# Kernel optimization log

Hardware: AMD Instinct MI355X
Metric: run time of the kernel (lower is better)

The kernel has to match this reference:

```python
import jax, jax.numpy as jnp
import numpy as np

EMBED = 1024
HEADS = 16
HEAD_DIM = EMBED // HEADS


def setup_inputs() -> dict:
    key = jax.random.key(0)
    ks = jax.random.split(key, 8)
    N, L = 4, 2048
    values = jax.random.normal(ks[0], (N, L, EMBED), dtype=jnp.float32)
    keys_ = jax.random.normal(ks[1], (N, L, EMBED), dtype=jnp.float32)
    queries = jax.random.normal(ks[2], (N, L, EMBED), dtype=jnp.float32)
    s = 1.0 / np.sqrt(HEAD_DIM)
    Wv = jax.random.normal(ks[3], (HEAD_DIM, HEAD_DIM), dtype=jnp.float32) * s
    Wk = jax.random.normal(ks[4], (HEAD_DIM, HEAD_DIM), dtype=jnp.float32) * s
    Wq = jax.random.normal(ks[5], (HEAD_DIM, HEAD_DIM), dtype=jnp.float32) * s
    Wo = jax.random.normal(ks[6], (EMBED, EMBED), dtype=jnp.float32) * (1.0 / np.sqrt(EMBED))
    bo = jnp.zeros((EMBED,), dtype=jnp.float32)
    return {"values": values, "keys": keys_, "queries": queries,
            "Wv": Wv, "Wk": Wk, "Wq": Wq, "Wo": Wo, "bo": bo}


def reference(values, keys, queries, Wv, Wk, Wq, Wo, bo):
    N, L, _ = queries.shape
    # split heads: [N, L, H, D]
    v = values.reshape(N, -1, HEADS, HEAD_DIM)
    k = keys.reshape(N, -1, HEADS, HEAD_DIM)
    q = queries.reshape(N, L, HEADS, HEAD_DIM)
    # per-head linear (same [D,D] weight shared across heads), torch Linear: x @ W.T
    v = jnp.einsum('nlhd,ed->nlhe', v, Wv)
    k = jnp.einsum('nlhd,ed->nlhe', k, Wk)
    q = jnp.einsum('nqhd,ed->nqhe', q, Wq)
    # attention scores [N, H, Q, K], scaled by sqrt(embed_size) as in source
    scores = jnp.einsum('nqhd,nkhd->nhqk', q, k) / jnp.sqrt(jnp.float32(EMBED))
    attn = jax.nn.softmax(scores, axis=-1)
    out = jnp.einsum('nhqk,nkhd->nqhd', attn, v).reshape(N, L, EMBED)
    return out @ Wo.T + bo
```

## Files before the change

### kernel.cpp

```cpp
#include <hip/hip_runtime.h>
#include <math.h>

#define EMBED 1024
#define HEADS 16
#define HD    64
#define NB    4
#define LSEQ  2048

typedef __attribute__((ext_vector_type(8))) short bf16x8;
typedef __attribute__((ext_vector_type(16))) float f32x16;

typedef __attribute__((address_space(1))) void as1_void;
typedef __attribute__((address_space(3))) void as3_void;

__device__ __forceinline__ void gload_lds16(const void* g, void* l) {
    __builtin_amdgcn_global_load_lds((const as1_void*)g, (as3_void*)l, 16, 0, 0);
}

__device__ inline bf16x8 as_bf16x8(uint4 u) {
    union { uint4 u; bf16x8 b; } c; c.u = u; return c.b;
}
__device__ inline unsigned short bf16r(float x) {
    unsigned u = __float_as_uint(x);
    u += 0x7fffu + ((u >> 16) & 1u);
    return (unsigned short)(u >> 16);
}
__device__ inline float bfh2f(unsigned short h) {
    return __uint_as_float(((unsigned)h) << 16);
}
__device__ inline void split2(float x, float y, unsigned& hw, unsigned& lw) {
    unsigned short hx = bf16r(x), hy = bf16r(y);
    unsigned short lx = bf16r(x - bfh2f(hx)), ly = bf16r(y - bfh2f(hy));
    hw = (unsigned)hx | ((unsigned)hy << 16);
    lw = (unsigned)lx | ((unsigned)ly << 16);
}

__global__ __launch_bounds__(256, 3) void proj_kernel(
    const float* __restrict__ Xv, const float* __restrict__ Xk, const float* __restrict__ Xq,
    const float* __restrict__ Wv, const float* __restrict__ Wk, const float* __restrict__ Wq,
    unsigned short* __restrict__ Vt, unsigned short* __restrict__ Kp, unsigned short* __restrict__ Qp)
{
    __shared__ uint4 sXh[128 * 8];
    __shared__ uint4 sXl[128 * 8];
    __shared__ uint4 sWh[64 * 8];
    __shared__ uint4 sWl[64 * 8];

    const int t = threadIdx.x;
    const int lane = t & 63, w = t >> 6;
    const int l5 = lane & 31, hi = lane >> 5;
    const int h  = blockIdx.y;
    const int n  = blockIdx.x >> 4;
    const int l0 = (blockIdx.x & 15) * 128;
    const int p  = blockIdx.z;

    const float QSC = 1.44269504088896341f / 32.0f;
    const float* Xp = (p == 0) ? Xv : (p == 1) ? Xk : Xq;
    const float* Wp = (p == 0) ? Wv : (p == 1) ? Wk : Wq;

    const int frow = t >> 4;
    const int fcol = t & 15;

    {
        const float* xb = Xp + ((size_t)(n * LSEQ + l0 + frow)) * EMBED + h * HD + fcol * 4;
        unsigned short* dh = (unsigned short*)sXh;
        unsigned short* dl = (unsigned short*)sXl;
        #pragma unroll
        for (int i = 0; i < 8; ++i) {
            int row = frow + i * 16;
            float4 v = *(const float4*)(xb + (size_t)i * 16 * EMBED);
            int gg = fcol >> 1, s8 = (fcol & 1) * 4;
            int idx = row * 64 + ((gg ^ (row & 7)) * 8) + s8;
            uint2 hv, lv;
            split2(v.x, v.y, hv.x, lv.x);
            split2(v.z, v.w, hv.y, lv.y);
            *(uint2*)(dh + idx) = hv;
            *(uint2*)(dl + idx) = lv;
        }
    }
    #pragma unroll
    for (int i = 0; i < 2; ++i) {
        int u = t + 256 * i;
        int e = u >> 3, g = u & 7;
        const float* wb = Wp + u * 8;
        float4 v0 = *(const float4*)(wb);
        float4 v1 = *(const float4*)(wb + 4);
        uint4 hq, lq;
        split2(v0.x, v0.y, hq.x, lq.x);
        split2(v0.z, v0.w, hq.y, lq.y);
        split2(v1.x, v1.y, hq.z, lq.z);
        split2(v1.z, v1.w, hq.w, lq.w);
        int idx = e * 8 + (g ^ (e & 7));
        sWh[idx] = hq;
        sWl[idx] = lq;
    }
    __syncthreads();

    f32x16 acc0, acc1;
    #pragma unroll
    for (int i = 0; i < 16; ++i) { acc0[i] = 0.f; acc1[i] = 0.f; }

    const int xrow = w * 32 + l5;
    const int w0r = l5, w1r = 32 + l5;
    #pragma unroll
    for (int kc = 0; kc < 4; ++kc) {
        int gsel = kc * 2 + hi;
        bf16x8 xh = as_bf16x8(sXh[xrow * 8 + (gsel ^ (xrow & 7))]);
        bf16x8 xl = as_bf16x8(sXl[xrow * 8 + (gsel ^ (xrow & 7))]);
        bf16x8 wh0 = as_bf16x8(sWh[w0r * 8 + (gsel ^ (w0r & 7))]);
        bf16x8 wl0 = as_bf16x8(sWl[w0r * 8 + (gsel ^ (w0r & 7))]);
        bf16x8 wh1 = as_bf16x8(sWh[w1r * 8 + (gsel ^ (w1r & 7))]);
        bf16x8 wl1 = as_bf16x8(sWl[w1r * 8 + (gsel ^ (w1r & 7))]);
        if (p == 0) {
            acc0 = __builtin_amdgcn_mfma_f32_32x32x16_bf16(wh0, xh, acc0, 0, 0, 0);
            acc0 = __builtin_amdgcn_mfma_f32_32x32x16_bf16(wh0, xl, acc0, 0, 0, 0);
            acc0 = __builtin_amdgcn_mfma_f32_32x32x16_bf16(wl0, xh, acc0, 0, 0, 0);
            acc1 = __builtin_amdgcn_mfma_f32_32x32x16_bf16(wh1, xh, acc1, 0, 0, 0);
            acc1 = __builtin_amdgcn_mfma_f32_32x32x16_bf16(wh1, xl, acc1, 0, 0, 0);
            acc1 = __builtin_amdgcn_mfma_f32_32x32x16_bf16(wl1, xh, acc1, 0, 0, 0);
        } else {
            acc0 = __builtin_amdgcn_mfma_f32_32x32x16_bf16(xh, wh0, acc0, 0, 0, 0);
            acc0 = __builtin_amdgcn_mfma_f32_32x32x16_bf16(xh, wl0, acc0, 0, 0, 0);
            acc0 = __builtin_amdgcn_mfma_f32_32x32x16_bf16(xl, wh0, acc0, 0, 0, 0);
            acc1 = __builtin_amdgcn_mfma_f32_32x32x16_bf16(xh, wh1, acc1, 0, 0, 0);
            acc1 = __builtin_amdgcn_mfma_f32_32x32x16_bf16(xh, wl1, acc1, 0, 0, 0);
            acc1 = __builtin_amdgcn_mfma_f32_32x32x16_bf16(xl, wh1, acc1, 0, 0, 0);
        }
    }

    if (p == 0) {
        unsigned short* vb = Vt + (((size_t)(n * HEADS + h)) * HD) * LSEQ + l0 + w * 32 + l5;
        #pragma unroll
        for (int r = 0; r < 16; ++r) {
            int er = (r & 3) + 8 * (r >> 2) + 4 * hi;
            vb[(size_t)er * LSEQ]        = bf16r(acc0[r]);
            vb[(size_t)(32 + er) * LSEQ] = bf16r(acc1[r]);
        }
    } else {
        unsigned short* dst = (p == 1) ? Kp : Qp;
        float sc = (p == 2) ? QSC : 1.0f;
        unsigned short* db = dst + (((size_t)(n * HEADS + h)) * LSEQ + l0 + w * 32) * HD;
        #pragma unroll
        for (int r = 0; r < 16; ++r) {
            int tok = (r & 3) + 8 * (r >> 2) + 4 * hi;
            db[(size_t)tok * HD + l5]      = bf16r(acc0[r] * sc);
            db[(size_t)tok * HD + 32 + l5] = bf16r(acc1[r] * sc);
        }
    }
}

__global__ __launch_bounds__(256, 4) void attn_kernel(
    const unsigned short* __restrict__ Qp, const unsigned short* __restrict__ Kp,
    const unsigned short* __restrict__ Vt,
    unsigned short* __restrict__ AOh, unsigned short* __restrict__ AOl)
{
    __shared__ uint4 sK[2][64 * 8];
    __shared__ uint4 sV[2][64 * 8];

    const int t = threadIdx.x;
    const int lane = t & 63, w = t >> 6;
    const int l5 = lane & 31, hi = lane >> 5;
    const int n = blockIdx.z, h = blockIdx.y;
    const int q0 = blockIdx.x * 128;
    const size_t hoff = ((size_t)n * HEADS + h) * (size_t)(LSEQ * HD);
    const unsigned short* Kh = Kp + hoff;
    const unsigned short* Vh = Vt + hoff;

    bf16x8 qf[4];
    {
        const uint4* qg = (const uint4*)(Qp + hoff + (size_t)(q0 + w * 32 + l5) * HD);
        #pragma unroll
        for (int kc = 0; kc < 4; ++kc) qf[kc] = as_bf16x8(qg[kc * 2 + hi]);
    }

    f32x16 Oa0, Oa1;
    #pragma unroll
    for (int i = 0; i < 16; ++i) { Oa0[i] = 0.f; Oa1[i] = 0.f; }
    float ls0 = 0.f, ls1 = 0.f;

    const int r0 = t >> 3;
    const int g0 = (t & 7) ^ (r0 & 7);
    const uint4* gK = (const uint4*)Kh;
    const uint4* gV = (const uint4*)Vh;

    #define STAGE(TILE, BUF)                                                        \
        do {                                                                        \
            int kb_ = (TILE) * 64;                                                  \
            gload_lds16(gK + (size_t)(kb_ + r0) * 8 + g0,        &sK[BUF][t]);      \
            gload_lds16(gK + (size_t)(kb_ + r0 + 32) * 8 + g0,   &sK[BUF][t + 256]);\
            gload_lds16(gV + (size_t)r0 * 256 + (kb_ >> 3) + g0, &sV[BUF][t]);      \
            gload_lds16(gV + (size_t)(r0 + 32) * 256 + (kb_ >> 3) + g0,             \
                        &sV[BUF][t + 256]);                                         \
        } while (0)

    STAGE(0, 0);
    int cur = 0;

    for (int tt = 0; tt < LSEQ / 64; ++tt) {
        if (tt + 1 < LSEQ / 64) {
            STAGE(tt + 1, cur ^ 1);
            asm volatile("s_waitcnt vmcnt(4)" ::: "memory");
        } else {
            asm volatile("s_waitcnt vmcnt(0)" ::: "memory");
        }
        __builtin_amdgcn_s_barrier();

        #pragma unroll
        for (int tc = 0; tc < 2; ++tc) {
            f32x16 c;
            #pragma unroll
            for (int i = 0; i < 16; ++i) c[i] = 0.f;
            int key = tc * 32 + l5;
            __builtin_amdgcn_s_setprio(1);
            #pragma unroll
            for (int kc = 0; kc < 4; ++kc) {
                bf16x8 kf = as_bf16x8(sK[cur][key * 8 + ((kc * 2 + hi) ^ (l5 & 7))]);
                c = __builtin_amdgcn_mfma_f32_32x32x16_bf16(kf, qf[kc], c, 0, 0, 0);
            }
            __builtin_amdgcn_s_setprio(0);

            unsigned pw[8];
            #pragma unroll
            for (int g = 0; g < 4; ++g) {
                float p0 = exp2f(c[4 * g]);
                float p1 = exp2f(c[4 * g + 1]);
                float p2 = exp2f(c[4 * g + 2]);
                float p3 = exp2f(c[4 * g + 3]);
                ls0 += (p0 + p1);
                ls1 += (p2 + p3);
                asm("v_cvt_pk_bf16_f32 %0, %1, %2" : "=v"(pw[2 * g])     : "v"(p0), "v"(p1));
                asm("v_cvt_pk_bf16_f32 %0, %1, %2" : "=v"(pw[2 * g + 1]) : "v"(p2), "v"(p3));
            }
            asm("v_permlane32_swap_b32 %0, %1" : "+v"(pw[0]), "+v"(pw[2]));
            asm("v_permlane32_swap_b32 %0, %1" : "+v"(pw[1]), "+v"(pw[3]));
            asm("v_permlane32_swap_b32 %0, %1" : "+v"(pw[4]), "+v"(pw[6]));
            asm("v_permlane32_swap_b32 %0, %1" : "+v"(pw[5]), "+v"(pw[7]));

            __builtin_amdgcn_s_setprio(1);
            #pragma unroll
            for (int win = 0; win < 2; ++win) {
                union { unsigned u[4]; bf16x8 b; } pf;
                pf.u[0] = pw[4 * win];
                pf.u[1] = pw[4 * win + 1];
                pf.u[2] = pw[4 * win + 2];
                pf.u[3] = pw[4 * win + 3];
                int vg = tc * 4 + (win << 1) + hi;
                bf16x8 v0 = as_bf16x8(sV[cur][ l5       * 8 + (vg ^ (l5 & 7))]);
                Oa0 = __builtin_amdgcn_mfma_f32_32x32x16_bf16(pf.b, v0, Oa0, 0, 0, 0);
                bf16x8 v1 = as_bf16x8(sV[cur][(32 + l5) * 8 + (vg ^ (l5 & 7))]);
                Oa1 = __builtin_amdgcn_mfma_f32_32x32x16_bf16(pf.b, v1, Oa1, 0, 0, 0);
            }
            __builtin_amdgcn_s_setprio(0);
        }
        __builtin_amdgcn_s_barrier();
        cur ^= 1;
    }
    #undef STAGE

    float lsum = ls0 + ls1;
    lsum += __shfl_xor(lsum, 32);
    float inv = 1.0f / lsum;
    float* sLf = (float*)&sK[0][0];
    if (hi == 0) sLf[w * 32 + l5] = inv;
    __syncthreads();

    unsigned short* hB = AOh + hoff;
    unsigned short* lB = AOl + hoff;
    #pragma unroll
    for (int r = 0; r < 16; ++r) {
        int qr = (r & 3) + 8 * (r >> 2) + 4 * hi;
        float invq = sLf[w * 32 + qr];
        size_t row = (size_t)(q0 + w * 32 + qr) * HD;
        float o0 = Oa0[r] * invq;
        float o1 = Oa1[r] * invq;
        unsigned short h0 = bf16r(o0), h1 = bf16r(o1);
        hB[row +      l5] = h0;
        hB[row + 32 + l5] = h1;
        lB[row +      l5] = bf16r(o0 - bfh2f(h0));
        lB[row + 32 + l5] = bf16r(o1 - bfh2f(h1));
    }
}

__global__ __launch_bounds__(256) void wsplit_kernel(
    const float* __restrict__ Wo,
    unsigned short* __restrict__ Woh, unsigned short* __restrict__ Wol)
{
    int i = blockIdx.x * 256 + threadIdx.x;
    float4 v = ((const float4*)Wo)[i];
    ushort4 h, l;
    h.x = bf16r(v.x); l.x = bf16r(v.x - bfh2f(h.x));
    h.y = bf16r(v.y); l.y = bf16r(v.y - bfh2f(h.y));
    h.z = bf16r(v.z); l.z = bf16r(v.z - bfh2f(h.z));
    h.w = bf16r(v.w); l.w = bf16r(v.w - bfh2f(h.w));
    ((ushort4*)Woh)[i] = h;
    ((ushort4*)Wol)[i] = l;
}

__global__ __launch_bounds__(256, 3) void outproj_kernel(
    const unsigned short* __restrict__ AOh, const unsigned short* __restrict__ AOl,
    const unsigned short* __restrict__ Woh, const unsigned short* __restrict__ Wol,
    const float* __restrict__ bo, float* __restrict__ out)
{
    __shared__ uint4 sAh[2][512];
    __shared__ uint4 sAl[2][512];
    __shared__ uint4 sBh[2][256];
    __shared__ uint4 sBl[2][256];

    const int t = threadIdx.x;
    const int lane = t & 63, w = t >> 6;
    const int l5 = lane & 31, hi = lane >> 5;
    const int m0 = blockIdx.x * 128;
    const int e0 = blockIdx.y * 64;
    const int n  = m0 >> 11, l0 = m0 & 2047;

    const int arow = t >> 2;
    const int aswz = (t & 3) ^ (arow & 3);

    #define OSTAGE(C, BUF)                                                            \
        do {                                                                          \
            int hh_ = (C) >> 1, hf_ = (C) & 1;                                        \
            const uint4* gAh_ = (const uint4*)(AOh) +                                 \
                (((size_t)n * HEADS + hh_) * LSEQ + l0) * 8 + hf_ * 4;                \
            const uint4* gAl_ = (const uint4*)(AOl) +                                 \
                (((size_t)n * HEADS + hh_) * LSEQ + l0) * 8 + hf_ * 4;                \
            const uint4* gBh_ = (const uint4*)(Woh) +                                 \
                (size_t)(e0 + arow) * 128 + hh_ * 8 + hf_ * 4;                        \
            const uint4* gBl_ = (const uint4*)(Wol) +                                 \
                (size_t)(e0 + arow) * 128 + hh_ * 8 + hf_ * 4;                        \
            gload_lds16(gAh_ + (size_t)arow * 8 + aswz,        &sAh[BUF][t]);         \
            gload_lds16(gAh_ + (size_t)(arow + 64) * 8 + aswz, &sAh[BUF][t + 256]);   \
            gload_lds16(gAl_ + (size_t)arow * 8 + aswz,        &sAl[BUF][t]);         \
            gload_lds16(gAl_ + (size_t)(arow + 64) * 8 + aswz, &sAl[BUF][t + 256]);   \
            gload_lds16(gBh_ + aswz, &sBh[BUF][t]);                                   \
            gload_lds16(gBl_ + aswz, &sBl[BUF][t]);                                   \
        } while (0)

    f32x16 acc0, acc1;
    #pragma unroll
    for (int i = 0; i < 16; ++i) { acc0[i] = 0.f; acc1[i] = 0.f; }

    OSTAGE(0, 0);
    int cur = 0;

    const int amr = w * 32 + l5;
    for (int c = 0; c < 32; ++c) {
        if (c + 1 < 32) {
            OSTAGE(c + 1, cur ^ 1);
            asm volatile("s_waitcnt vmcnt(6)" ::: "memory");
        } else {
            asm volatile("s_waitcnt vmcnt(0)" ::: "memory");
        }
        __builtin_amdgcn_s_barrier();

        __builtin_amdgcn_s_setprio(1);
        #pragma unroll
        for (int ks = 0; ks < 2; ++ks) {
            int gx = ks * 2 + hi;
            bf16x8 ah = as_bf16x8(sAh[cur][amr * 4 + (gx ^ (amr & 3))]);
            bf16x8 al = as_bf16x8(sAl[cur][amr * 4 + (gx ^ (amr & 3))]);
            bf16x8 bh0 = as_bf16x8(sBh[cur][ l5       * 4 + (gx ^ (l5 & 3))]);
            bf16x8 bh1 = as_bf16x8(sBh[cur][(32 + l5) * 4 + (gx ^ (l5 & 3))]);
            bf16x8 bl0 = as_bf16x8(sBl[cur][ l5       * 4 + (gx ^ (l5 & 3))]);
            bf16x8 bl1 = as_bf16x8(sBl[cur][(32 + l5) * 4 + (gx ^ (l5 & 3))]);

            acc0 = __builtin_amdgcn_mfma_f32_32x32x16_bf16(ah, bh0, acc0, 0, 0, 0);
            acc1 = __builtin_amdgcn_mfma_f32_32x32x16_bf16(ah, bh1, acc1, 0, 0, 0);
            acc0 = __builtin_amdgcn_mfma_f32_32x32x16_bf16(ah, bl0, acc0, 0, 0, 0);
            acc1 = __builtin_amdgcn_mfma_f32_32x32x16_bf16(ah, bl1, acc1, 0, 0, 0);
            acc0 = __builtin_amdgcn_mfma_f32_32x32x16_bf16(al, bh0, acc0, 0, 0, 0);
            acc1 = __builtin_amdgcn_mfma_f32_32x32x16_bf16(al, bh1, acc1, 0, 0, 0);
        }
        __builtin_amdgcn_s_setprio(0);
        __builtin_amdgcn_s_barrier();
        cur ^= 1;
    }
    #undef OSTAGE

    float b0 = bo[e0 + l5];
    float b1 = bo[e0 + 32 + l5];
    #pragma unroll
    for (int r = 0; r < 16; ++r) {
        int row = m0 + w * 32 + (r & 3) + 8 * (r >> 2) + 4 * hi;
        float* o = out + (size_t)row * EMBED + e0;
        o[l5]      = acc0[r] + b0;
        o[32 + l5] = acc1[r] + b1;
    }
}

extern "C" void kernel_launch(void* const* d_in, const int* in_sizes, int n_in,
                              void* d_out, int out_size, void* d_ws, size_t ws_size,
                              hipStream_t stream)
{
    const float* values  = (const float*)d_in[0];
    const float* keys    = (const float*)d_in[1];
    const float* queries = (const float*)d_in[2];
    const float* Wv      = (const float*)d_in[3];
    const float* Wk      = (const float*)d_in[4];
    const float* Wq      = (const float*)d_in[5];
    const float* Wo      = (const float*)d_in[6];
    const float* bo      = (const float*)d_in[7];
    float* out = (float*)d_out;

    const size_t bufElems = (size_t)NB * HEADS * LSEQ * HD;
    unsigned short* Qp  = (unsigned short*)d_ws;
    unsigned short* Kp  = Qp  + bufElems;
    unsigned short* Vt  = Kp  + bufElems;
    unsigned short* AOh = Vt  + bufElems;
    unsigned short* AOl = AOh + bufElems;
    unsigned short* Woh = AOl + bufElems;
    unsigned short* Wol = Woh + (size_t)EMBED * EMBED;

    wsplit_kernel<<<dim3(1024), 256, 0, stream>>>(Wo, Woh, Wol);
    proj_kernel<<<dim3(NB * 16, HEADS, 3), 256, 0, stream>>>(values, keys, queries, Wv, Wk, Wq, Vt, Kp, Qp);
    attn_kernel<<<dim3(LSEQ / 128, HEADS, NB), 256, 0, stream>>>(Qp, Kp, Vt, AOh, AOl);
    outproj_kernel<<<dim3(NB * LSEQ / 128, EMBED / 64), 256, 0, stream>>>(AOh, AOl, Woh, Wol, bo, out);
}
```

Before: 352.5 us.

## Fold Wo split into proj kernel and remap attn/outproj blocks per XCD

Removes the separate wsplit kernel launch by adding a fourth z-slice to the projection grid that converts Wo into bf16 hi/lo halves. Also remaps block indices in the attention and output-projection kernels so consecutive blocks dispatched to the same XCD share a head or row tile, which is meant to improve L2 reuse of K/V and A tiles. It saves one launch. It risks extra, mostly idle blocks in the projection grid and depends on the assumed round-robin dispatch of blocks across XCDs.

```diff
diff --git a/kernel.cpp b/kernel.cpp
--- a/kernel.cpp
+++ b/kernel.cpp
@@ -38,7 +38,9 @@
 __global__ __launch_bounds__(256, 3) void proj_kernel(
     const float* __restrict__ Xv, const float* __restrict__ Xk, const float* __restrict__ Xq,
     const float* __restrict__ Wv, const float* __restrict__ Wk, const float* __restrict__ Wq,
-    unsigned short* __restrict__ Vt, unsigned short* __restrict__ Kp, unsigned short* __restrict__ Qp)
+    const float* __restrict__ Wo,
+    unsigned short* __restrict__ Vt, unsigned short* __restrict__ Kp, unsigned short* __restrict__ Qp,
+    unsigned short* __restrict__ Woh, unsigned short* __restrict__ Wol)
 {
     __shared__ uint4 sXh[128 * 8];
     __shared__ uint4 sXl[128 * 8];
@@ -46,6 +48,21 @@
     __shared__ uint4 sWl[64 * 8];
 
     const int t = threadIdx.x;
+
+    if (blockIdx.z == 3) {
+        int w_id = blockIdx.x + blockIdx.y * 64;
+        int i = w_id * 256 + t;
+        float4 v = ((const float4*)Wo)[i];
+        ushort4 h4, l4;
+        h4.x = bf16r(v.x); l4.x = bf16r(v.x - bfh2f(h4.x));
+        h4.y = bf16r(v.y); l4.y = bf16r(v.y - bfh2f(h4.y));
+        h4.z = bf16r(v.z); l4.z = bf16r(v.z - bfh2f(h4.z));
+        h4.w = bf16r(v.w); l4.w = bf16r(v.w - bfh2f(h4.w));
+        ((ushort4*)Woh)[i] = h4;
+        ((ushort4*)Wol)[i] = l4;
+        return;
+    }
+
     const int lane = t & 63, w = t >> 6;
     const int l5 = lane & 31, hi = lane >> 5;
     const int h  = blockIdx.y;
@@ -159,8 +176,13 @@
     const int t = threadIdx.x;
     const int lane = t & 63, w = t >> 6;
     const int l5 = lane & 31, hi = lane >> 5;
-    const int n = blockIdx.z, h = blockIdx.y;
-    const int q0 = blockIdx.x * 128;
+
+    const int b   = blockIdx.x + blockIdx.y * 16 + blockIdx.z * 256;
+    const int xcd = b & 7, u = b >> 3;
+    const int grp = xcd * 8 + (u >> 4);
+    const int n   = grp >> 4, h = grp & 15;
+    const int q0  = (u & 15) * 128;
+
     const size_t hoff = ((size_t)n * HEADS + h) * (size_t)(LSEQ * HD);
     const unsigned short* Kh = Kp + hoff;
     const unsigned short* Vh = Vt + hoff;
@@ -280,21 +302,6 @@
     }
 }
 
-__global__ __launch_bounds__(256) void wsplit_kernel(
-    const float* __restrict__ Wo,
-    unsigned short* __restrict__ Woh, unsigned short* __restrict__ Wol)
-{
-    int i = blockIdx.x * 256 + threadIdx.x;
-    float4 v = ((const float4*)Wo)[i];
-    ushort4 h, l;
-    h.x = bf16r(v.x); l.x = bf16r(v.x - bfh2f(h.x));
-    h.y = bf16r(v.y); l.y = bf16r(v.y - bfh2f(h.y));
-    h.z = bf16r(v.z); l.z = bf16r(v.z - bfh2f(h.z));
-    h.w = bf16r(v.w); l.w = bf16r(v.w - bfh2f(h.w));
-    ((ushort4*)Woh)[i] = h;
-    ((ushort4*)Wol)[i] = l;
-}
-
 __global__ __launch_bounds__(256, 3) void outproj_kernel(
     const unsigned short* __restrict__ AOh, const unsigned short* __restrict__ AOl,
     const unsigned short* __restrict__ Woh, const unsigned short* __restrict__ Wol,
@@ -308,9 +315,12 @@
     const int t = threadIdx.x;
     const int lane = t & 63, w = t >> 6;
     const int l5 = lane & 31, hi = lane >> 5;
-    const int m0 = blockIdx.x * 128;
-    const int e0 = blockIdx.y * 64;
-    const int n  = m0 >> 11, l0 = m0 & 2047;
+
+    const int bl  = blockIdx.x + blockIdx.y * 64;
+    const int xcd = bl & 7, u = bl >> 3;
+    const int m0  = (xcd * 8 + (u & 7)) * 128;
+    const int e0  = (u >> 3) * 64;
+    const int n   = m0 >> 11, l0 = m0 & 2047;
 
     const int arow = t >> 2;
     const int aswz = (t & 3) ^ (arow & 3);
@@ -409,8 +419,8 @@
     unsigned short* Woh = AOl + bufElems;
     unsigned short* Wol = Woh + (size_t)EMBED * EMBED;
 
-    wsplit_kernel<<<dim3(1024), 256, 0, stream>>>(Wo, Woh, Wol);
-    proj_kernel<<<dim3(NB * 16, HEADS, 3), 256, 0, stream>>>(values, keys, queries, Wv, Wk, Wq, Vt, Kp, Qp);
+    proj_kernel<<<dim3(NB * 16, HEADS, 4), 256, 0, stream>>>(
+        values, keys, queries, Wv, Wk, Wq, Wo, Vt, Kp, Qp, Woh, Wol);
     attn_kernel<<<dim3(LSEQ / 128, HEADS, NB), 256, 0, stream>>>(Qp, Kp, Vt, AOh, AOl);
     outproj_kernel<<<dim3(NB * LSEQ / 128, EMBED / 64), 256, 0, stream>>>(AOh, AOl, Woh, Wol, bo, out);
 }
```

After: 349.9 us. About the same (-0.7%).
